# Kernel tuning notes

Hardware: AMD Instinct MI355X
Metric: run time of the kernel (lower is better)

## Reference

```python
import jax, jax.numpy as jnp
import numpy as np

SUP = 7
EPS = 1e-12

def _gather(t, idx):
    # t: (b, v, d), idx: (b, v, n) -> (b, v, n, d)
    return jax.vmap(lambda tb, ib: tb[ib])(t, idx)

def _knn(v, k):
    # squared pairwise distance, exclude self (smallest), return k neighbors
    q = jnp.sum(v * v, axis=-1)
    d = q[:, :, None] + q[:, None, :] - 2.0 * jnp.einsum('bid,bjd->bij', v, v)
    _, idx = jax.lax.top_k(-d, k + 1)
    return idx[:, :, 1:]

def _dir_norm(v, idx):
    d = _gather(v, idx) - v[:, :, None, :]
    n = jnp.sqrt(jnp.sum(d * d, axis=-1, keepdims=True))
    return d / jnp.maximum(n, EPS)

def _col_norm(d):
    n = jnp.sqrt(jnp.sum(d * d, axis=0, keepdims=True))
    return d / jnp.maximum(n, EPS)

def _conv_surface(idx, v, directions, kernel_num):
    theta = jax.nn.silu(_dir_norm(v, idx) @ _col_norm(directions))  # (b,V,n,SUP*K)
    b, V, n, _ = theta.shape
    theta = theta.reshape(b, V, n, SUP, kernel_num)
    return jnp.sum(jnp.max(theta, axis=2), axis=2)

def _conv_layer(idx, v, fm, W, bias, directions, out_c):
    b, V, n = idx.shape
    theta = jax.nn.silu(_dir_norm(v, idx) @ _col_norm(directions))  # (b,V,n,SUP*out_c)
    feat = fm @ W + bias                                             # (b,V,(SUP+1)*out_c)
    center = feat[:, :, :out_c]
    support = _gather(feat[:, :, out_c:], idx)                       # (b,V,n,SUP*out_c)
    act = (theta * support).reshape(b, V, n, SUP, out_c)
    act = jnp.sum(jnp.max(act, axis=2), axis=2)
    return center + act

def _bn(x, g, b, eps=1e-5):
    # BatchNorm1d in training mode: stats over batch and vertex dims
    m = jnp.mean(x, axis=(0, 1))
    var = jnp.var(x, axis=(0, 1))
    return (x - m) / jnp.sqrt(var + eps) * g + b

def _nearest(target, source):
    d = (jnp.sum(source * source, -1)[:, None, :] + jnp.sum(target * target, -1)[:, :, None]
         - 2.0 * jnp.einsum('bid,bjd->bij', target, source))
    return jnp.argmin(d, axis=-1)  # (b, v1)

def _forward(x, d0, w1, b1, dir1, g1, bb1, w2, b2, dir2, g2, bb2,
             w3, b3, dir3, g3, bb3, w4, b4, dir4, perm1, perm2):
    nb = _knn(x, 10)
    fm0 = jax.nn.silu(_conv_surface(nb, x, d0, 128))
    fm1 = jax.nn.silu(_bn(_conv_layer(nb, x, fm0, w1, b1, dir1, 128), g1, bb1))
    # pool 1: max over 4-NN features, then subsample to V/4
    pooled = jnp.max(_gather(fm1, _knn(x, 4)), axis=2)
    v1 = x[:, perm1]
    f1 = pooled[:, perm1]
    nb = _knn(v1, 10)
    fm2 = jax.nn.silu(_bn(_conv_layer(nb, v1, f1, w2, b2, dir2, 256), g2, bb2))
    fm3 = jax.nn.silu(_bn(_conv_layer(nb, v1, fm2, w3, b3, dir3, 256), g3, bb3))
    # pool 2
    pooled = jnp.max(_gather(fm3, _knn(v1, 4)), axis=2)
    v2 = v1[:, perm2]
    f2 = pooled[:, perm2]
    nb = _knn(v2, 10)
    fm4 = _conv_layer(nb, v2, f2, w4, b4, dir4, 512)
    n1 = _nearest(x, v1)
    n2 = _nearest(x, v2)
    up = lambda f, i: jax.vmap(lambda fb, ib: fb[ib])(f, i)
    return jnp.concatenate([fm0, fm1, up(fm2, n1), up(fm3, n1), up(fm4, n2)], axis=-1)

def setup_inputs() -> dict:
    key = jax.random.key(0)
    ks = jax.random.split(key, 24)
    B, V = 2, 4096
    uni = lambda k, shape, s: jax.random.uniform(k, shape, jnp.float32, -s, s)
    s1 = (128 * (SUP + 1)) ** -0.5
    s2 = (256 * (SUP + 1)) ** -0.5
    s4 = (512 * (SUP + 1)) ** -0.5
    s0 = (SUP * 128) ** -0.5
    inp = {
        'x': jax.random.normal(ks[0], (B, V, 3), jnp.float32),
        'd0': uni(ks[1], (3, SUP * 128), s0),
        'w1': uni(ks[2], (128, (SUP + 1) * 128), s1),
        'b1': uni(ks[3], ((SUP + 1) * 128,), s1),
        'dir1': uni(ks[4], (3, SUP * 128), s1),
        'g1': jnp.ones((128,), jnp.float32),
        'bb1': jnp.zeros((128,), jnp.float32),
        'w2': uni(ks[5], (128, (SUP + 1) * 256), s2),
        'b2': uni(ks[6], ((SUP + 1) * 256,), s2),
        'dir2': uni(ks[7], (3, SUP * 256), s2),
        'g2': jnp.ones((256,), jnp.float32),
        'bb2': jnp.zeros((256,), jnp.float32),
        'w3': uni(ks[8], (256, (SUP + 1) * 256), s2),
        'b3': uni(ks[9], ((SUP + 1) * 256,), s2),
        'dir3': uni(ks[10], (3, SUP * 256), s2),
        'g3': jnp.ones((256,), jnp.float32),
        'bb3': jnp.zeros((256,), jnp.float32),
        'w4': uni(ks[11], (256, (SUP + 1) * 512), s4),
        'b4': uni(ks[12], ((SUP + 1) * 512,), s4),
        'dir4': uni(ks[13], (3, SUP * 512), s4),
        'perm1': jax.random.permutation(ks[20], V)[: V // 4].astype(jnp.int32),
        'perm2': jax.random.permutation(ks[21], V // 4)[: V // 16].astype(jnp.int32),
    }
    return inp

def reference(x, d0, w1, b1, dir1, g1, bb1, w2, b2, dir2, g2, bb2,
              w3, b3, dir3, g3, bb3, w4, b4, dir4, perm1, perm2):
    return _forward(x, d0, w1, b1, dir1, g1, bb1, w2, b2, dir2, g2, bb2,
                    w3, b3, dir3, g3, bb3, w4, b4, dir4, perm1, perm2)
```

## Files before the change

kernel.cpp:

```cpp
#include <hip/hip_runtime.h>
#include <math.h>
#include <float.h>
#include <limits.h>

#define BNUM 2
#define V0 4096
#define V1N 1024
#define V2N 256
#define SUPN 7

typedef float float4v __attribute__((ext_vector_type(4)));
typedef float float2v __attribute__((ext_vector_type(2)));
typedef unsigned short ushort4v __attribute__((ext_vector_type(4)));
typedef unsigned long long u64;

__device__ __forceinline__ float fast_silu(float x){
  return __fdividef(x, 1.0f + __expf(-x));
}

__device__ __forceinline__ unsigned short f2bf(float f){
  unsigned int u=__float_as_uint(f);
  u += 0x7FFFu + ((u>>16)&1u);
  return (unsigned short)(u>>16);
}
__device__ __forceinline__ float bf2f(unsigned short h){
  return __uint_as_float(((unsigned int)h)<<16);
}

__device__ __forceinline__ unsigned int fkey(float f){
  unsigned int u = __float_as_uint(f);
  int m = ((int)u) >> 31;
  return u ^ (unsigned int)(m | 0x80000000);
}

__device__ __forceinline__ u64 shfl_xor_u64(u64 v, int m){
  unsigned int lo = (unsigned int)v, hi = (unsigned int)(v>>32);
  lo = (unsigned int)__shfl_xor((int)lo, m);
  hi = (unsigned int)__shfl_xor((int)hi, m);
  return ((u64)hi<<32) | lo;
}

__global__ void colnorm_all_k(const float* __restrict__ d0, const float* __restrict__ dir1,
                              const float* __restrict__ dir2, const float* __restrict__ dir3,
                              const float* __restrict__ dir4,
                              float* __restrict__ cn0, float* __restrict__ cn1,
                              float* __restrict__ cn2, float* __restrict__ cn3,
                              float* __restrict__ cn4, float* __restrict__ stats){
  int c = blockIdx.x*256 + threadIdx.x;
  if(c < 1280) stats[c] = 0.0f;
  const float* s; float* o; int nc;
  if(c < 896){ s=d0; o=cn0; nc=896; }
  else if((c-=896) < 896){ s=dir1; o=cn1; nc=896; }
  else if((c-=896) < 1792){ s=dir2; o=cn2; nc=1792; }
  else if((c-=1792) < 1792){ s=dir3; o=cn3; nc=1792; }
  else { c-=1792; if(c>=3584) return; s=dir4; o=cn4; nc=3584; }
  float a=s[c], b=s[nc+c], e=s[2*nc+c];
  float n=sqrtf(a*a+b*b+e*e); n=fmaxf(n,1e-12f);
  o[c]=a/n; o[nc+c]=b/n; o[2*nc+c]=e/n;
}

template<int VC, int THREADS, int MINW>
__global__ __launch_bounds__(THREADS, MINW) void knn10_k(const float* __restrict__ pts,
    int* __restrict__ out_idx, float* __restrict__ out_dirn)
{
  constexpr int CHUNK = VC/64;
  constexpr int QPB = THREADS/64;
  __shared__ float4v sp4[VC];
  __shared__ float sdd[QPB][34];
  __shared__ int   sdi[QPB][34];
  int t = threadIdx.x;
  int lane = t & 63;
  int wv   = t >> 6;
  int b = blockIdx.y;
  int j = blockIdx.x*QPB + wv;
  const float* pb = pts + (size_t)b*VC*3;
  for(int i=t; i<VC; i+=THREADS){
    float x=pb[3*i], y=pb[3*i+1], z=pb[3*i+2];
    float4v v; v[0]=x; v[1]=y; v[2]=z; v[3]=x*x+y*y+z*z;
    sp4[i]=v;
  }
  __syncthreads();
  float qx=pb[3*j], qy=pb[3*j+1], qz=pb[3*j+2];
  float qs=qx*qx+qy*qy+qz*qz;

  float dc[CHUNK];
  float p0=INFINITY, p1=INFINITY, p2=INFINITY, p3=INFINITY;
  #pragma unroll
  for(int c=0;c<CHUNK;c++){
    float4v p = sp4[c*64+lane];
    float dot = qx*p[0]+qy*p[1]+qz*p[2];
    float d = fmaf(-2.0f, dot, p[3]+qs);
    dc[c]=d;
    float s=d, a;
    a=fminf(p0,s); s=fmaxf(p0,s); p0=a;
    a=fminf(p1,s); s=fmaxf(p1,s); p1=a;
    a=fminf(p2,s); s=fmaxf(p2,s); p2=a;
    p3=fminf(p3,s);
  }

  float prev=-INFINITY;
  for(int sel=0; sel<11; ++sel){
    float cand = p0>prev ? p0 : (p1>prev ? p1 : (p2>prev ? p2 : (p3>prev ? p3 : INFINITY)));
    #pragma unroll
    for(int s=32;s;s>>=1) cand = fminf(cand, __shfl_xor(cand, s));
    prev=cand;
  }
  float v11 = prev;

  int cnt=0;
  #pragma unroll
  for(int c=0;c<CHUNK;c++){
    bool hit = dc[c] <= v11;
    u64 m = __ballot(hit);
    if(m){
      if(hit){
        int pos = cnt + __popcll(m & ((1ull<<lane)-1ull));
        if(pos<32){ sdd[wv][pos]=dc[c]; sdi[wv][pos]=c*64+lane; }
      }
      cnt += (int)__popcll(m);
    }
  }
  if(cnt>32) cnt=32;

  if(lane < cnt){
    float dl = sdd[wv][lane]; int il = sdi[wv][lane];
    int rank=0;
    for(int m2=0;m2<cnt;m2++){
      float dm=sdd[wv][m2]; int im=sdi[wv][m2];
      rank += (dm<dl || (dm==dl && im<il)) ? 1 : 0;
    }
    if(rank>=1 && rank<=10){
      size_t obase=((size_t)b*VC+j)*10 + (rank-1);
      out_idx[obase]=il;
      float4v p = sp4[il];
      float dx=p[0]-qx, dy=p[1]-qy, dz=p[2]-qz;
      float n=sqrtf(dx*dx+dy*dy+dz*dz); n=fmaxf(n,1e-12f);
      out_dirn[obase*3]=dx/n; out_dirn[obase*3+1]=dy/n; out_dirn[obase*3+2]=dz/n;
    }
  }
}

__global__ __launch_bounds__(512) void nearest_both_k(
    const float* __restrict__ v1, const float* __restrict__ v2,
    const float* __restrict__ x,
    int* __restrict__ n1, int* __restrict__ n2)
{
  __shared__ float4v s1[V1N];
  __shared__ float4v s2[V2N];
  int t=threadIdx.x;
  int lane=t&63, wv=t>>6;
  int b=blockIdx.y; int j=blockIdx.x*8+wv;
  const float* c1=v1+(size_t)b*V1N*3;
  const float* c2=v2+(size_t)b*V2N*3;
  for(int i=t;i<V1N;i+=512){
    float xx=c1[3*i],yy=c1[3*i+1],zz=c1[3*i+2];
    float4v v; v[0]=xx;v[1]=yy;v[2]=zz;v[3]=xx*xx+yy*yy+zz*zz; s1[i]=v;
  }
  for(int i=t;i<V2N;i+=512){
    float xx=c2[3*i],yy=c2[3*i+1],zz=c2[3*i+2];
    float4v v; v[0]=xx;v[1]=yy;v[2]=zz;v[3]=xx*xx+yy*yy+zz*zz; s2[i]=v;
  }
  __syncthreads();
  const float* qb=x+(size_t)b*V0*3;
  float qx=qb[3*j],qy=qb[3*j+1],qz=qb[3*j+2];
  float qs=qx*qx+qy*qy+qz*qz;
  u64 bk=~0ull;
  #pragma unroll 4
  for(int c=0;c<V1N/64;c++){
    int i=c*64+lane;
    float4v p=s1[i];
    float dot=qx*p[0]+qy*p[1]+qz*p[2];
    float d=fmaf(-2.0f,dot,p[3]+qs);
    u64 k=((u64)fkey(d)<<32)|(unsigned int)i;
    bk = k<bk ? k : bk;
  }
  #pragma unroll
  for(int s=32;s;s>>=1){ u64 o=shfl_xor_u64(bk,s); bk = o<bk?o:bk; }
  if(lane==0) n1[(size_t)b*V0+j]=(int)(bk&0xffffffffu);
  bk=~0ull;
  #pragma unroll 4
  for(int c=0;c<V2N/64;c++){
    int i=c*64+lane;
    float4v p=s2[i];
    float dot=qx*p[0]+qy*p[1]+qz*p[2];
    float d=fmaf(-2.0f,dot,p[3]+qs);
    u64 k=((u64)fkey(d)<<32)|(unsigned int)i;
    bk = k<bk ? k : bk;
  }
  #pragma unroll
  for(int s=32;s;s>>=1){ u64 o=shfl_xor_u64(bk,s); bk = o<bk?o:bk; }
  if(lane==0) n2[(size_t)b*V0+j]=(int)(bk&0xffffffffu);
}

template<int NODES>
__global__ __launch_bounds__(64*NODES) void conv_surf_k(
    const float* __restrict__ dirn, const float* __restrict__ cnd,
    float* __restrict__ fm0, float* __restrict__ outbuf)
{
  int tid=threadIdx.x, nd=tid>>6, t=tid&63;
  int b=blockIdx.y, i=blockIdx.x*NODES+nd;
  __shared__ float sd[NODES][32];
  if(t<30) sd[nd][t]=dirn[((size_t)(b*V0+i))*30+t];
  __syncthreads();
  float acc0=0.0f, acc1=0.0f;
  for(int s=0;s<SUPN;s++){
    int col=s*128+t;
    float wa0=cnd[col],     wa1=cnd[896+col],     wa2=cnd[1792+col];
    float wb0=cnd[col+64],  wb1=cnd[896+col+64],  wb2=cnd[1792+col+64];
    float m0=-INFINITY, m1=-INFINITY;
    #pragma unroll
    for(int n=0;n<10;n++){
      float dx=sd[nd][3*n], dy=sd[nd][3*n+1], dz=sd[nd][3*n+2];
      m0=fmaxf(m0, fast_silu(dx*wa0+dy*wa1+dz*wa2));
      m1=fmaxf(m1, fast_silu(dx*wb0+dy*wb1+dz*wb2));
    }
    acc0+=m0; acc1+=m1;
  }
  float r0=fast_silu(acc0), r1=fast_silu(acc1);
  size_t frow=(size_t)(b*V0+i)*128;
  fm0[frow+t]=r0; fm0[frow+64+t]=r1;
  size_t orow=(size_t)(b*V0+i)*1280;
  outbuf[orow+t]=r0; outbuf[orow+64+t]=r1;
}

__global__ __launch_bounds__(256) void gemm_split_k(
    const float* __restrict__ A, const float* __restrict__ W,
    const float* __restrict__ bias,
    float* __restrict__ Cc, unsigned short* __restrict__ Sp,
    int M, int N, int K, int outC)
{
  __shared__ float As[16][132];
  __shared__ float Bs[16][132];
  int t=threadIdx.x;
  int tx=t&15, ty=t>>4;
  int bm=blockIdx.y*128, bn=blockIdx.x*128;
  float4v acc[2][2][4];
  #pragma unroll
  for(int a=0;a<2;a++)
    #pragma unroll
    for(int bidx=0;bidx<2;bidx++)
      #pragma unroll
      for(int m=0;m<4;m++) acc[a][bidx][m]=(float4v)(0.0f);
  int arow=t>>2, akk=(t&3)*4;
  int brow=t>>4, bcol=(t&15)*4;
  for(int k0=0;k0<K;k0+=16){
    float4v a0=*(const float4v*)&A[(size_t)(bm+arow)*K    + k0+akk];
    float4v a1=*(const float4v*)&A[(size_t)(bm+64+arow)*K + k0+akk];
    float4v b0=*(const float4v*)&W[(size_t)(k0+brow)*N + bn+bcol];
    float4v b1=*(const float4v*)&W[(size_t)(k0+brow)*N + bn+64+bcol];
    __syncthreads();
    #pragma unroll
    for(int u=0;u<4;u++){ As[akk+u][arow]=a0[u]; As[akk+u][64+arow]=a1[u]; }
    *(float4v*)&Bs[brow][bcol]=b0;
    *(float4v*)&Bs[brow][64+bcol]=b1;
    __syncthreads();
    #pragma unroll
    for(int kk=0;kk<16;kk++){
      float4v alo=*(const float4v*)&As[kk][ty*4];
      float4v ahi=*(const float4v*)&As[kk][64+ty*4];
      float4v blo=*(const float4v*)&Bs[kk][tx*4];
      float4v bhi=*(const float4v*)&Bs[kk][64+tx*4];
      #pragma unroll
      for(int mi=0;mi<4;mi++){
        acc[0][0][mi] += alo[mi]*blo;
        acc[0][1][mi] += alo[mi]*bhi;
        acc[1][0][mi] += ahi[mi]*blo;
        acc[1][1][mi] += ahi[mi]*bhi;
      }
    }
  }
  float4v bl=*(const float4v*)&bias[bn+tx*4];
  float4v bh=*(const float4v*)&bias[bn+64+tx*4];
  if(bn + 128 <= outC){
    #pragma unroll
    for(int mh=0;mh<2;mh++)
      #pragma unroll
      for(int mi=0;mi<4;mi++){
        size_t row=(size_t)(bm+mh*64+ty*4+mi);
        *(float4v*)&Cc[row*outC + bn+tx*4]    = acc[mh][0][mi]+bl;
        *(float4v*)&Cc[row*outC + bn+64+tx*4] = acc[mh][1][mi]+bh;
      }
  } else {
    int sw = 7*outC;
    int scol = bn - outC;
    #pragma unroll
    for(int mh=0;mh<2;mh++)
      #pragma unroll
      for(int mi=0;mi<4;mi++){
        size_t row=(size_t)(bm+mh*64+ty*4+mi);
        float4v r0=acc[mh][0][mi]+bl, r1=acc[mh][1][mi]+bh;
        ushort4v p0,p1;
        #pragma unroll
        for(int u=0;u<4;u++){ p0[u]=f2bf(r0[u]); p1[u]=f2bf(r1[u]); }
        *(ushort4v*)&Sp[row*sw + scol+tx*4]    = p0;
        *(ushort4v*)&Sp[row*sw + scol+64+tx*4] = p1;
      }
  }
}

template<int C, int TPN, int NODES>
__global__ __launch_bounds__(TPN*NODES) void conv_agg_k(
    const float* __restrict__ cent, const unsigned short* __restrict__ sup,
    int Vb,
    const float* __restrict__ dirn, const int* __restrict__ nbidx,
    const float* __restrict__ cnd,
    float* __restrict__ outp, float* __restrict__ stats)
{
  constexpr int ncol = SUPN*C;
  constexpr int NT = TPN*NODES;
  int tid=threadIdx.x, nd=tid/TPN, t=tid%TPN;
  int b=blockIdx.y, i=blockIdx.x*NODES+nd;
  __shared__ float sd[NODES][32];
  __shared__ int snb[NODES][12];
  __shared__ float ssum[C], ssq[C];
  if(t<30) sd[nd][t]=dirn[((size_t)(b*Vb+i))*30+t];
  if(t<10) snb[nd][t]=nbidx[(size_t)(b*Vb+i)*10+t];
  for(int c=tid;c<C;c+=NT){ ssum[c]=0.0f; ssq[c]=0.0f; }
  __syncthreads();
  float acc[4];
  {
    float4v cv=*(const float4v*)&cent[(size_t)(b*Vb+i)*C + t*4];
    #pragma unroll
    for(int v=0;v<4;v++) acc[v]=cv[v];
  }
  const unsigned short* fb=sup+(size_t)b*Vb*ncol;
  for(int s=0;s<SUPN;s++){
    int colbase = s*C + t*4;
    float w0[4],w1[4],w2[4],m[4];
    #pragma unroll
    for(int v=0;v<4;v++){
      w0[v]=cnd[colbase+v]; w1[v]=cnd[ncol+colbase+v]; w2[v]=cnd[2*ncol+colbase+v];
      m[v]=-INFINITY;
    }
    #pragma unroll
    for(int n=0;n<10;n++){
      float dx=sd[nd][3*n],dy=sd[nd][3*n+1],dz=sd[nd][3*n+2];
      ushort4v sv=*(const ushort4v*)&fb[(size_t)snb[nd][n]*ncol + colbase];
      #pragma unroll
      for(int v=0;v<4;v++){
        float d=dx*w0[v]+dy*w1[v]+dz*w2[v];
        m[v]=fmaxf(m[v], fast_silu(d)*bf2f(sv[v]));
      }
    }
    #pragma unroll
    for(int v=0;v<4;v++) acc[v]+=m[v];
  }
  {
    float4v ov;
    #pragma unroll
    for(int v=0;v<4;v++) ov[v]=acc[v];
    *(float4v*)&outp[(size_t)(b*Vb+i)*C + t*4]=ov;
  }
  if(stats){
    #pragma unroll
    for(int v=0;v<4;v++){
      atomicAdd(&ssum[t*4+v], acc[v]);
      atomicAdd(&ssq[t*4+v], acc[v]*acc[v]);
    }
    __syncthreads();
    for(int c=tid;c<C;c+=NT){
      atomicAdd(&stats[c], ssum[c]);
      atomicAdd(&stats[C+c], ssq[c]);
    }
  }
}

__global__ void bn_silu_k(const float* __restrict__ xin, const float* __restrict__ sums,
                          float invM, int C, const float* __restrict__ g, const float* __restrict__ bb,
                          float* __restrict__ y, int nquad, float* __restrict__ osl, int cshift)
{
  int gid=blockIdx.x*blockDim.x+threadIdx.x;
  if(gid>=nquad) return;
  int base=gid*4;
  int c=base&(C-1);
  float4v xv=*(const float4v*)&xin[base];
  float4v sm=*(const float4v*)&sums[c];
  float4v sq=*(const float4v*)&sums[C+c];
  float4v gv=*(const float4v*)&g[c];
  float4v bv=*(const float4v*)&bb[c];
  float4v r;
  #pragma unroll
  for(int u=0;u<4;u++){
    float mean=sm[u]*invM;
    float var=sq[u]*invM - mean*mean;
    float v=(xv[u]-mean)*rsqrtf(var+1e-5f)*gv[u]+bv[u];
    r[u]=fast_silu(v);
  }
  *(float4v*)&y[base]=r;
  if(osl){
    int row=base>>cshift;
    *(float4v*)&osl[(size_t)row*1280 + c]=r;
  }
}

template<int C, int NODES>
__global__ __launch_bounds__((C/4)*NODES) void pool_gather_k(
    const float* __restrict__ fm, int Vsrc,
    const int* __restrict__ idx10, const int* __restrict__ perm,
    const float* __restrict__ vsrc,
    float* __restrict__ fout, float* __restrict__ vout, int Vq)
{
  constexpr int TPN=C/4;
  int tid=threadIdx.x, nd=tid/TPN, t=tid%TPN;
  int b=blockIdx.y, j=blockIdx.x*NODES+nd;
  int r=perm[j];
  const int* id=idx10+((size_t)b*Vsrc+r)*10;
  const float* fb=fm+(size_t)b*Vsrc*C;
  float4v m=(float4v)(-INFINITY);
  #pragma unroll
  for(int n=0;n<4;n++){
    float4v fv=*(const float4v*)&fb[(size_t)id[n]*C + t*4];
    #pragma unroll
    for(int u=0;u<4;u++) m[u]=fmaxf(m[u],fv[u]);
  }
  *(float4v*)&fout[(size_t)(b*Vq+j)*C + t*4]=m;
  if(t<3) vout[((size_t)b*Vq+j)*3+t]=vsrc[((size_t)b*Vsrc+r)*3+t];
}

__global__ __launch_bounds__(256) void concat_k(
    const float* __restrict__ fm2, const float* __restrict__ fm3,
    const float* __restrict__ fm4,
    const int* __restrict__ n1, const int* __restrict__ n2,
    float* __restrict__ outp)
{
  int b=blockIdx.y, i=blockIdx.x, t=threadIdx.x;
  int j1=n1[b*V0+i], j2=n2[b*V0+i];
  float4v v;
  if(t<64)       v = ((const float4v*)(fm2 + ((size_t)b*V1N+j1)*256))[t];
  else if(t<128) v = ((const float4v*)(fm3 + ((size_t)b*V1N+j1)*256))[t-64];
  else           v = ((const float4v*)(fm4 + ((size_t)b*V2N+j2)*512))[t-128];
  ((float4v*)(outp + (size_t)(b*V0+i)*1280))[64+t] = v;
}

extern "C" void kernel_launch(void* const* d_in, const int* in_sizes, int n_in,
                              void* d_out, int out_size, void* d_ws, size_t ws_size,
                              hipStream_t stream) {
  const float* x   =(const float*)d_in[0];
  const float* d0  =(const float*)d_in[1];
  const float* w1  =(const float*)d_in[2];
  const float* b1  =(const float*)d_in[3];
  const float* dir1=(const float*)d_in[4];
  const float* g1  =(const float*)d_in[5];
  const float* bb1 =(const float*)d_in[6];
  const float* w2  =(const float*)d_in[7];
  const float* b2  =(const float*)d_in[8];
  const float* dir2=(const float*)d_in[9];
  const float* g2  =(const float*)d_in[10];
  const float* bb2 =(const float*)d_in[11];
  const float* w3  =(const float*)d_in[12];
  const float* b3  =(const float*)d_in[13];
  const float* dir3=(const float*)d_in[14];
  const float* g3  =(const float*)d_in[15];
  const float* bb3 =(const float*)d_in[16];
  const float* w4  =(const float*)d_in[17];
  const float* b4  =(const float*)d_in[18];
  const float* dir4=(const float*)d_in[19];
  const int* perm1 =(const int*)d_in[20];
  const int* perm2 =(const int*)d_in[21];
  float* out=(float*)d_out;

  float* w=(float*)d_ws;
  size_t off=0;
  auto alloc=[&](size_t n){ float* p=w+off; off+=n; return p; };
  float* cn0 =alloc(2688);
  float* cn1 =alloc(2688);
  float* cn2 =alloc(5376);
  float* cn3 =alloc(5376);
  float* cn4 =alloc(10752);
  float* dirnx =alloc((size_t)BNUM*V0*30);
  float* dirnv1=alloc((size_t)BNUM*V1N*30);
  float* dirnv2=alloc((size_t)BNUM*V2N*30);
  float* fm0 =alloc((size_t)BNUM*V0*128);
  float* cent=alloc((size_t)BNUM*V0*128);
  unsigned short* supb=(unsigned short*)alloc((size_t)BNUM*V0*896/2);
  float* fm1r=alloc((size_t)BNUM*V0*128);
  float* fm1 =alloc((size_t)BNUM*V0*128);
  float* f1  =alloc((size_t)BNUM*V1N*128);
  float* v1  =alloc((size_t)BNUM*V1N*3);
  float* fm2r=alloc((size_t)BNUM*V1N*256);
  float* fm2 =alloc((size_t)BNUM*V1N*256);
  float* fm3r=alloc((size_t)BNUM*V1N*256);
  float* fm3 =alloc((size_t)BNUM*V1N*256);
  float* f2  =alloc((size_t)BNUM*V2N*256);
  float* v2  =alloc((size_t)BNUM*V2N*3);
  float* fm4 =alloc((size_t)BNUM*V2N*512);
  float* stats=alloc(1280);
  int* idx10x =(int*)alloc((size_t)BNUM*V0*10);
  int* idx10v1=(int*)alloc((size_t)BNUM*V1N*10);
  int* idx10v2=(int*)alloc((size_t)BNUM*V2N*10);
  int* n1i =(int*)alloc((size_t)BNUM*V0);
  int* n2i =(int*)alloc((size_t)BNUM*V0);

  colnorm_all_k<<<dim3(35),256,0,stream>>>(d0,dir1,dir2,dir3,dir4,cn0,cn1,cn2,cn3,cn4,stats);

  knn10_k<V0,1024,4><<<dim3(V0/16,BNUM),1024,0,stream>>>(x, idx10x, dirnx);
  conv_surf_k<4><<<dim3(V0/4,BNUM),256,0,stream>>>(dirnx, cn0, fm0, out);

  gemm_split_k<<<dim3(1024/128,(BNUM*V0)/128),256,0,stream>>>(fm0, w1, b1, cent, supb, BNUM*V0, 1024, 128, 128);
  conv_agg_k<128,32,8><<<dim3(V0/8,BNUM),256,0,stream>>>(cent, supb, V0, dirnx, idx10x, cn1, fm1r, stats);
  bn_silu_k<<<dim3((BNUM*V0*128/4)/256),256,0,stream>>>(fm1r, stats, 1.0f/(BNUM*V0), 128, g1, bb1, fm1, BNUM*V0*128/4, out+128, 7);

  pool_gather_k<128,8><<<dim3(V1N/8,BNUM),256,0,stream>>>(fm1, V0, idx10x, perm1, x, f1, v1, V1N);

  knn10_k<V1N,256,6><<<dim3(V1N/4,BNUM),256,0,stream>>>(v1, idx10v1, dirnv1);

  gemm_split_k<<<dim3(2048/128,(BNUM*V1N)/128),256,0,stream>>>(f1, w2, b2, cent, supb, BNUM*V1N, 2048, 128, 256);
  conv_agg_k<256,64,4><<<dim3(V1N/4,BNUM),256,0,stream>>>(cent, supb, V1N, dirnv1, idx10v1, cn2, fm2r, stats+256);
  bn_silu_k<<<dim3((BNUM*V1N*256/4)/256),256,0,stream>>>(fm2r, stats+256, 1.0f/(BNUM*V1N), 256, g2, bb2, fm2, BNUM*V1N*256/4, nullptr, 8);

  gemm_split_k<<<dim3(2048/128,(BNUM*V1N)/128),256,0,stream>>>(fm2, w3, b3, cent, supb, BNUM*V1N, 2048, 256, 256);
  conv_agg_k<256,64,4><<<dim3(V1N/4,BNUM),256,0,stream>>>(cent, supb, V1N, dirnv1, idx10v1, cn3, fm3r, stats+768);
  bn_silu_k<<<dim3((BNUM*V1N*256/4)/256),256,0,stream>>>(fm3r, stats+768, 1.0f/(BNUM*V1N), 256, g3, bb3, fm3, BNUM*V1N*256/4, nullptr, 8);

  pool_gather_k<256,4><<<dim3(V2N/4,BNUM),256,0,stream>>>(fm3, V1N, idx10v1, perm2, v1, f2, v2, V2N);

  knn10_k<V2N,256,6><<<dim3(V2N/4,BNUM),256,0,stream>>>(v2, idx10v2, dirnv2);

  gemm_split_k<<<dim3(4096/128,(BNUM*V2N)/128),256,0,stream>>>(f2, w4, b4, cent, supb, BNUM*V2N, 4096, 256, 512);
  conv_agg_k<512,128,2><<<dim3(V2N/2,BNUM),256,0,stream>>>(cent, supb, V2N, dirnv2, idx10v2, cn4, fm4, nullptr);

  nearest_both_k<<<dim3(V0/8,BNUM),512,0,stream>>>(v1, v2, x, n1i, n2i);

  concat_k<<<dim3(V0,BNUM),256,0,stream>>>(fm2, fm3, fm4, n1i, n2i, out);
}
```

Measured before the change: 521.8 us.

## Split conv aggregation neighbors across half-waves with prefetched support loads

Rewrites the conv aggregation kernel so that each node is handled by twice as many threads. The two halves of a 64-wide wave each take 5 of the 10 neighbors, and their per-support maxima are combined with a cross-lane shuffle. Support-feature loads for the next support slot are double-buffered in registers, and the direction weights are loaded as float4 vectors. The aim is more memory-level parallelism and latency hiding for the gather-bound aggregation, at the cost of more blocks, redundant weight loads, and extra shuffle work.

```diff
diff --git a/kernel.cpp b/kernel.cpp
--- a/kernel.cpp
+++ b/kernel.cpp
@@ -298,8 +298,8 @@
   }
 }
 
-template<int C, int TPN, int NODES>
-__global__ __launch_bounds__(TPN*NODES) void conv_agg_k(
+template<int C, int NODES>
+__global__ __launch_bounds__(NODES*(C/2)) void conv_agg_k(
     const float* __restrict__ cent, const unsigned short* __restrict__ sup,
     int Vb,
     const float* __restrict__ dirn, const int* __restrict__ nbidx,
@@ -307,55 +307,86 @@
     float* __restrict__ outp, float* __restrict__ stats)
 {
   constexpr int ncol = SUPN*C;
-  constexpr int NT = TPN*NODES;
-  int tid=threadIdx.x, nd=tid/TPN, t=tid%TPN;
+  constexpr int NT = NODES*(C/2);
+  constexpr int WPN = C/128;
+  int tid=threadIdx.x;
+  int lane = tid & 63;
+  int wvid = tid >> 6;
+  int nd = wvid / WPN;
+  int wn = wvid % WPN;
+  int tcg = (lane & 31) + wn*32;
+  int h = lane >> 5;
+  int ln = tid & (C/2 - 1);
   int b=blockIdx.y, i=blockIdx.x*NODES+nd;
   __shared__ float sd[NODES][32];
   __shared__ int snb[NODES][12];
   __shared__ float ssum[C], ssq[C];
-  if(t<30) sd[nd][t]=dirn[((size_t)(b*Vb+i))*30+t];
-  if(t<10) snb[nd][t]=nbidx[(size_t)(b*Vb+i)*10+t];
-  for(int c=tid;c<C;c+=NT){ ssum[c]=0.0f; ssq[c]=0.0f; }
+  if(ln<30) sd[nd][ln]=dirn[((size_t)(b*Vb+i))*30+ln];
+  if(ln<10) snb[nd][ln]=nbidx[(size_t)(b*Vb+i)*10+ln];
+  if(stats) for(int c=tid;c<C;c+=NT){ ssum[c]=0.0f; ssq[c]=0.0f; }
   __syncthreads();
+
+  unsigned int off[5];
+  float ndx[5], ndy[5], ndz[5];
+  #pragma unroll
+  for(int n=0;n<5;n++){
+    int nn = h*5+n;
+    off[n] = (unsigned int)snb[nd][nn]*ncol + tcg*4;
+    ndx[n]=sd[nd][3*nn]; ndy[n]=sd[nd][3*nn+1]; ndz[n]=sd[nd][3*nn+2];
+  }
+  const unsigned short* fb = sup + (size_t)b*Vb*ncol;
+
   float acc[4];
   {
-    float4v cv=*(const float4v*)&cent[(size_t)(b*Vb+i)*C + t*4];
+    float4v cv=*(const float4v*)&cent[(size_t)(b*Vb+i)*C + tcg*4];
     #pragma unroll
     for(int v=0;v<4;v++) acc[v]=cv[v];
   }
-  const unsigned short* fb=sup+(size_t)b*Vb*ncol;
+
+  ushort4v buf[2][5];
+  #pragma unroll
+  for(int n=0;n<5;n++) buf[0][n] = *(const ushort4v*)&fb[off[n]];
+
+  #pragma unroll
   for(int s=0;s<SUPN;s++){
-    int colbase = s*C + t*4;
-    float w0[4],w1[4],w2[4],m[4];
+    if(s+1<SUPN){
+      #pragma unroll
+      for(int n=0;n<5;n++) buf[(s+1)&1][n] = *(const ushort4v*)&fb[off[n] + (s+1)*C];
+    }
+    int colbase = s*C + tcg*4;
+    float4v w0=*(const float4v*)&cnd[colbase];
+    float4v w1=*(const float4v*)&cnd[ncol+colbase];
+    float4v w2=*(const float4v*)&cnd[2*ncol+colbase];
+    float m[4]={-INFINITY,-INFINITY,-INFINITY,-INFINITY};
+    #pragma unroll
+    for(int n=0;n<5;n++){
+      ushort4v sv = buf[s&1][n];
+      #pragma unroll
+      for(int v=0;v<4;v++){
+        float d = ndx[n]*w0[v] + ndy[n]*w1[v] + ndz[n]*w2[v];
+        m[v] = fmaxf(m[v], fast_silu(d)*bf2f(sv[v]));
+      }
+    }
     #pragma unroll
     for(int v=0;v<4;v++){
-      w0[v]=cnd[colbase+v]; w1[v]=cnd[ncol+colbase+v]; w2[v]=cnd[2*ncol+colbase+v];
-      m[v]=-INFINITY;
-    }
-    #pragma unroll
-    for(int n=0;n<10;n++){
-      float dx=sd[nd][3*n],dy=sd[nd][3*n+1],dz=sd[nd][3*n+2];
-      ushort4v sv=*(const ushort4v*)&fb[(size_t)snb[nd][n]*ncol + colbase];
+      m[v] = fmaxf(m[v], __shfl_xor(m[v], 32));
+      acc[v] += m[v];
+    }
+  }
+
+  if(h==0){
+    float4v ov;
+    #pragma unroll
+    for(int v=0;v<4;v++) ov[v]=acc[v];
+    *(float4v*)&outp[(size_t)(b*Vb+i)*C + tcg*4]=ov;
+  }
+  if(stats){
+    if(h==0){
       #pragma unroll
       for(int v=0;v<4;v++){
-        float d=dx*w0[v]+dy*w1[v]+dz*w2[v];
-        m[v]=fmaxf(m[v], fast_silu(d)*bf2f(sv[v]));
+        atomicAdd(&ssum[tcg*4+v], acc[v]);
+        atomicAdd(&ssq[tcg*4+v], acc[v]*acc[v]);
       }
-    }
-    #pragma unroll
-    for(int v=0;v<4;v++) acc[v]+=m[v];
-  }
-  {
-    float4v ov;
-    #pragma unroll
-    for(int v=0;v<4;v++) ov[v]=acc[v];
-    *(float4v*)&outp[(size_t)(b*Vb+i)*C + t*4]=ov;
-  }
-  if(stats){
-    #pragma unroll
-    for(int v=0;v<4;v++){
-      atomicAdd(&ssum[t*4+v], acc[v]);
-      atomicAdd(&ssq[t*4+v], acc[v]*acc[v]);
     }
     __syncthreads();
     for(int c=tid;c<C;c+=NT){
@@ -497,7 +528,7 @@
   conv_surf_k<4><<<dim3(V0/4,BNUM),256,0,stream>>>(dirnx, cn0, fm0, out);
 
   gemm_split_k<<<dim3(1024/128,(BNUM*V0)/128),256,0,stream>>>(fm0, w1, b1, cent, supb, BNUM*V0, 1024, 128, 128);
-  conv_agg_k<128,32,8><<<dim3(V0/8,BNUM),256,0,stream>>>(cent, supb, V0, dirnx, idx10x, cn1, fm1r, stats);
+  conv_agg_k<128,4><<<dim3(V0/4,BNUM),256,0,stream>>>(cent, supb, V0, dirnx, idx10x, cn1, fm1r, stats);
   bn_silu_k<<<dim3((BNUM*V0*128/4)/256),256,0,stream>>>(fm1r, stats, 1.0f/(BNUM*V0), 128, g1, bb1, fm1, BNUM*V0*128/4, out+128, 7);
 
   pool_gather_k<128,8><<<dim3(V1N/8,BNUM),256,0,stream>>>(fm1, V0, idx10x, perm1, x, f1, v1, V1N);
@@ -505,11 +536,11 @@
   knn10_k<V1N,256,6><<<dim3(V1N/4,BNUM),256,0,stream>>>(v1, idx10v1, dirnv1);
 
   gemm_split_k<<<dim3(2048/128,(BNUM*V1N)/128),256,0,stream>>>(f1, w2, b2, cent, supb, BNUM*V1N, 2048, 128, 256);
-  conv_agg_k<256,64,4><<<dim3(V1N/4,BNUM),256,0,stream>>>(cent, supb, V1N, dirnv1, idx10v1, cn2, fm2r, stats+256);
+  conv_agg_k<256,2><<<dim3(V1N/2,BNUM),256,0,stream>>>(cent, supb, V1N, dirnv1, idx10v1, cn2, fm2r, stats+256);
   bn_silu_k<<<dim3((BNUM*V1N*256/4)/256),256,0,stream>>>(fm2r, stats+256, 1.0f/(BNUM*V1N), 256, g2, bb2, fm2, BNUM*V1N*256/4, nullptr, 8);
 
   gemm_split_k<<<dim3(2048/128,(BNUM*V1N)/128),256,0,stream>>>(fm2, w3, b3, cent, supb, BNUM*V1N, 2048, 256, 256);
-  conv_agg_k<256,64,4><<<dim3(V1N/4,BNUM),256,0,stream>>>(cent, supb, V1N, dirnv1, idx10v1, cn3, fm3r, stats+768);
+  conv_agg_k<256,2><<<dim3(V1N/2,BNUM),256,0,stream>>>(cent, supb, V1N, dirnv1, idx10v1, cn3, fm3r, stats+768);
   bn_silu_k<<<dim3((BNUM*V1N*256/4)/256),256,0,stream>>>(fm3r, stats+768, 1.0f/(BNUM*V1N), 256, g3, bb3, fm3, BNUM*V1N*256/4, nullptr, 8);
 
   pool_gather_k<256,4><<<dim3(V2N/4,BNUM),256,0,stream>>>(fm3, V1N, idx10v1, perm2, v1, f2, v2, V2N);
@@ -517,7 +548,7 @@
   knn10_k<V2N,256,6><<<dim3(V2N/4,BNUM),256,0,stream>>>(v2, idx10v2, dirnv2);
 
   gemm_split_k<<<dim3(4096/128,(BNUM*V2N)/128),256,0,stream>>>(f2, w4, b4, cent, supb, BNUM*V2N, 4096, 256, 512);
-  conv_agg_k<512,128,2><<<dim3(V2N/2,BNUM),256,0,stream>>>(cent, supb, V2N, dirnv2, idx10v2, cn4, fm4, nullptr);
+  conv_agg_k<512,1><<<dim3(V2N,BNUM),256,0,stream>>>(cent, supb, V2N, dirnv2, idx10v2, cn4, fm4, nullptr);
 
   nearest_both_k<<<dim3(V0/8,BNUM),512,0,stream>>>(v1, v2, x, n1i, n2i);
 
```

Result: slower. 564.3 us (+8.1%).

## Swap conv aggregation loop order and double-buffer neighbor gathers

Applied to the files above, without the earlier changes.

Reorders the conv aggregation kernel so the outer loop runs over neighbors and the inner loop over all support slots, keeping per-slot running maxima in registers. Neighbor feature rows are prefetched into two register buffers so the next neighbor's gather overlaps compute on the current one. Direction weights are staged into shared memory once per block, and stats shared memory is zeroed only when stats are needed. This trades more registers and a larger shared-memory footprint (3*7*C floats) for more memory-level parallelism, which may reduce occupancy for large C.

```diff
diff --git a/kernel.cpp b/kernel.cpp
--- a/kernel.cpp
+++ b/kernel.cpp
@@ -313,49 +313,95 @@
   __shared__ float sd[NODES][32];
   __shared__ int snb[NODES][12];
   __shared__ float ssum[C], ssq[C];
+  __shared__ float scn[3*ncol];
   if(t<30) sd[nd][t]=dirn[((size_t)(b*Vb+i))*30+t];
   if(t<10) snb[nd][t]=nbidx[(size_t)(b*Vb+i)*10+t];
-  for(int c=tid;c<C;c+=NT){ ssum[c]=0.0f; ssq[c]=0.0f; }
+  for(int c=tid;c<3*ncol;c+=NT) scn[c]=cnd[c];
+  if(stats) for(int c=tid;c<C;c+=NT){ ssum[c]=0.0f; ssq[c]=0.0f; }
   __syncthreads();
+
+  const int col0 = t*4;
+  const unsigned short* fb = sup + (size_t)b*Vb*ncol;
+
+  float m[SUPN][4];
+  #pragma unroll
+  for(int s=0;s<SUPN;s++)
+    #pragma unroll
+    for(int v=0;v<4;v++) m[s][v]=-INFINITY;
+
+  ushort4v bufA[SUPN], bufB[SUPN];
+  float dax,day,daz, dbx,dby,dbz;
+  {
+    unsigned int off=(unsigned int)snb[nd][0]*ncol + col0;
+    #pragma unroll
+    for(int s=0;s<SUPN;s++) bufA[s]=*(const ushort4v*)&fb[off + s*C];
+    dax=sd[nd][0]; day=sd[nd][1]; daz=sd[nd][2];
+  }
+  #pragma unroll 1
+  for(int np=0;np<5;np++){
+    {
+      int nn=2*np+1;
+      unsigned int off=(unsigned int)snb[nd][nn]*ncol + col0;
+      #pragma unroll
+      for(int s=0;s<SUPN;s++) bufB[s]=*(const ushort4v*)&fb[off + s*C];
+      dbx=sd[nd][3*nn]; dby=sd[nd][3*nn+1]; dbz=sd[nd][3*nn+2];
+    }
+    #pragma unroll
+    for(int s=0;s<SUPN;s++){
+      int cb=s*C+col0;
+      float4v w0=*(const float4v*)&scn[cb];
+      float4v w1=*(const float4v*)&scn[ncol+cb];
+      float4v w2=*(const float4v*)&scn[2*ncol+cb];
+      ushort4v sv=bufA[s];
+      #pragma unroll
+      for(int v=0;v<4;v++){
+        float d = dax*w0[v] + day*w1[v] + daz*w2[v];
+        m[s][v] = fmaxf(m[s][v], fast_silu(d)*bf2f(sv[v]));
+      }
+    }
+    if(np<4){
+      int nn=2*np+2;
+      unsigned int off=(unsigned int)snb[nd][nn]*ncol + col0;
+      #pragma unroll
+      for(int s=0;s<SUPN;s++) bufA[s]=*(const ushort4v*)&fb[off + s*C];
+      dax=sd[nd][3*nn]; day=sd[nd][3*nn+1]; daz=sd[nd][3*nn+2];
+    }
+    #pragma unroll
+    for(int s=0;s<SUPN;s++){
+      int cb=s*C+col0;
+      float4v w0=*(const float4v*)&scn[cb];
+      float4v w1=*(const float4v*)&scn[ncol+cb];
+      float4v w2=*(const float4v*)&scn[2*ncol+cb];
+      ushort4v sv=bufB[s];
+      #pragma unroll
+      for(int v=0;v<4;v++){
+        float d = dbx*w0[v] + dby*w1[v] + dbz*w2[v];
+        m[s][v] = fmaxf(m[s][v], fast_silu(d)*bf2f(sv[v]));
+      }
+    }
+  }
+
   float acc[4];
   {
-    float4v cv=*(const float4v*)&cent[(size_t)(b*Vb+i)*C + t*4];
-    #pragma unroll
-    for(int v=0;v<4;v++) acc[v]=cv[v];
-  }
-  const unsigned short* fb=sup+(size_t)b*Vb*ncol;
-  for(int s=0;s<SUPN;s++){
-    int colbase = s*C + t*4;
-    float w0[4],w1[4],w2[4],m[4];
+    float4v cv=*(const float4v*)&cent[(size_t)(b*Vb+i)*C + col0];
     #pragma unroll
     for(int v=0;v<4;v++){
-      w0[v]=cnd[colbase+v]; w1[v]=cnd[ncol+colbase+v]; w2[v]=cnd[2*ncol+colbase+v];
-      m[v]=-INFINITY;
-    }
-    #pragma unroll
-    for(int n=0;n<10;n++){
-      float dx=sd[nd][3*n],dy=sd[nd][3*n+1],dz=sd[nd][3*n+2];
-      ushort4v sv=*(const ushort4v*)&fb[(size_t)snb[nd][n]*ncol + colbase];
-      #pragma unroll
-      for(int v=0;v<4;v++){
-        float d=dx*w0[v]+dy*w1[v]+dz*w2[v];
-        m[v]=fmaxf(m[v], fast_silu(d)*bf2f(sv[v]));
-      }
-    }
-    #pragma unroll
-    for(int v=0;v<4;v++) acc[v]+=m[v];
+      acc[v]=cv[v];
+      #pragma unroll
+      for(int s=0;s<SUPN;s++) acc[v]+=m[s][v];
+    }
   }
   {
     float4v ov;
     #pragma unroll
     for(int v=0;v<4;v++) ov[v]=acc[v];
-    *(float4v*)&outp[(size_t)(b*Vb+i)*C + t*4]=ov;
+    *(float4v*)&outp[(size_t)(b*Vb+i)*C + col0]=ov;
   }
   if(stats){
     #pragma unroll
     for(int v=0;v<4;v++){
-      atomicAdd(&ssum[t*4+v], acc[v]);
-      atomicAdd(&ssq[t*4+v], acc[v]*acc[v]);
+      atomicAdd(&ssum[col0+v], acc[v]);
+      atomicAdd(&ssq[col0+v], acc[v]*acc[v]);
     }
     __syncthreads();
     for(int c=tid;c<C;c+=NT){
```

Result: faster. 491.9 us (-5.7%).

## Double-buffer neighbor gathers and stage direction weights in shared memory in conv_agg

Applied to the files above, without the earlier changes.

Rewrites the support-point loop in the conv aggregation kernel as a software pipeline with two register buffers, so the gathers for the next support point are issued before the current one is computed. It also copies the normalized direction matrix into shared memory once per block and reads it as float4, replacing scalar global loads. Neighbor offsets are precomputed once. This aims to hide gather latency, at the cost of higher register pressure from the 20 ushort4 buffers and more shared memory use per block, which could lower occupancy.

```diff
diff --git a/kernel.cpp b/kernel.cpp
--- a/kernel.cpp
+++ b/kernel.cpp
@@ -313,49 +313,77 @@
   __shared__ float sd[NODES][32];
   __shared__ int snb[NODES][12];
   __shared__ float ssum[C], ssq[C];
+  __shared__ float scn[3*ncol];
   if(t<30) sd[nd][t]=dirn[((size_t)(b*Vb+i))*30+t];
   if(t<10) snb[nd][t]=nbidx[(size_t)(b*Vb+i)*10+t];
-  for(int c=tid;c<C;c+=NT){ ssum[c]=0.0f; ssq[c]=0.0f; }
+  for(int c=tid;c<3*ncol;c+=NT) scn[c]=cnd[c];
+  if(stats) for(int c=tid;c<C;c+=NT){ ssum[c]=0.0f; ssq[c]=0.0f; }
   __syncthreads();
+
+  const int col0 = t*4;
+  const unsigned short* fb = sup + (size_t)b*Vb*ncol;
+
+  unsigned int off[10];
+  #pragma unroll
+  for(int n=0;n<10;n++) off[n]=(unsigned int)snb[nd][n]*ncol + col0;
+
   float acc[4];
   {
-    float4v cv=*(const float4v*)&cent[(size_t)(b*Vb+i)*C + t*4];
+    float4v cv=*(const float4v*)&cent[(size_t)(b*Vb+i)*C + col0];
     #pragma unroll
     for(int v=0;v<4;v++) acc[v]=cv[v];
   }
-  const unsigned short* fb=sup+(size_t)b*Vb*ncol;
-  for(int s=0;s<SUPN;s++){
-    int colbase = s*C + t*4;
-    float w0[4],w1[4],w2[4],m[4];
-    #pragma unroll
-    for(int v=0;v<4;v++){
-      w0[v]=cnd[colbase+v]; w1[v]=cnd[ncol+colbase+v]; w2[v]=cnd[2*ncol+colbase+v];
-      m[v]=-INFINITY;
-    }
-    #pragma unroll
-    for(int n=0;n<10;n++){
-      float dx=sd[nd][3*n],dy=sd[nd][3*n+1],dz=sd[nd][3*n+2];
-      ushort4v sv=*(const ushort4v*)&fb[(size_t)snb[nd][n]*ncol + colbase];
-      #pragma unroll
-      for(int v=0;v<4;v++){
-        float d=dx*w0[v]+dy*w1[v]+dz*w2[v];
-        m[v]=fmaxf(m[v], fast_silu(d)*bf2f(sv[v]));
-      }
-    }
-    #pragma unroll
-    for(int v=0;v<4;v++) acc[v]+=m[v];
-  }
+
+#define LSTEP(BUF, SS) { \
+    unsigned int so=(unsigned int)(SS)*C; \
+    _Pragma("unroll") \
+    for(int n=0;n<10;n++) BUF[n]=*(const ushort4v*)&fb[off[n]+so]; \
+  }
+#define CSTEP(BUF, SS) { \
+    int cb=(SS)*C+col0; \
+    float4v w0=*(const float4v*)&scn[cb]; \
+    float4v w1=*(const float4v*)&scn[ncol+cb]; \
+    float4v w2=*(const float4v*)&scn[2*ncol+cb]; \
+    float mm[4]={-INFINITY,-INFINITY,-INFINITY,-INFINITY}; \
+    _Pragma("unroll") \
+    for(int n=0;n<10;n++){ \
+      float dx=sd[nd][3*n], dy=sd[nd][3*n+1], dz=sd[nd][3*n+2]; \
+      ushort4v sv=BUF[n]; \
+      _Pragma("unroll") \
+      for(int v=0;v<4;v++){ \
+        float d=dx*w0[v]+dy*w1[v]+dz*w2[v]; \
+        mm[v]=fmaxf(mm[v], fast_silu(d)*bf2f(sv[v])); \
+      } \
+    } \
+    _Pragma("unroll") \
+    for(int v=0;v<4;v++) acc[v]+=mm[v]; \
+  }
+
+  ushort4v bufA[10], bufB[10];
+  LSTEP(bufA, 0)
+  #pragma unroll 1
+  for(int k=0;k<3;k++){
+    int s=2*k;
+    LSTEP(bufB, s+1)
+    CSTEP(bufA, s)
+    LSTEP(bufA, s+2)
+    CSTEP(bufB, s+1)
+  }
+  CSTEP(bufA, 6)
+#undef LSTEP
+#undef CSTEP
+
   {
     float4v ov;
     #pragma unroll
     for(int v=0;v<4;v++) ov[v]=acc[v];
-    *(float4v*)&outp[(size_t)(b*Vb+i)*C + t*4]=ov;
+    *(float4v*)&outp[(size_t)(b*Vb+i)*C + col0]=ov;
   }
   if(stats){
     #pragma unroll
     for(int v=0;v<4;v++){
-      atomicAdd(&ssum[t*4+v], acc[v]);
-      atomicAdd(&ssq[t*4+v], acc[v]*acc[v]);
+      atomicAdd(&ssum[col0+v], acc[v]);
+      atomicAdd(&ssq[col0+v], acc[v]*acc[v]);
     }
     __syncthreads();
     for(int c=tid;c<C;c+=NT){
```

After: 563.9 us. +8.1%, slower.
